# Kernel optimization log

Hardware: AMD Instinct MI355X
Metric: run time of the kernel (lower is better)

Reference implementation:

```python
import jax, jax.numpy as jnp
import numpy as np

INPUT_DIM = 1024
HIDDEN_DIM = 64  # per-head dim
NUM_HEADS = 16
LN_EPS = 1e-5


def setup_inputs() -> dict:
    key = jax.random.key(0)
    ks = jax.random.split(key, 12)
    B, S, D = 2, 2048, INPUT_DIM
    HD = HIDDEN_DIM * NUM_HEADS
    s_in = 1.0 / np.sqrt(D)
    s_hd = 1.0 / np.sqrt(HD)
    return {
        "x": jax.random.normal(ks[0], (B, S, D), dtype=jnp.float32),
        "Wq": jax.random.normal(ks[1], (D, HD), dtype=jnp.float32) * s_in,
        "bq": jax.random.normal(ks[2], (HD,), dtype=jnp.float32) * 0.02,
        "Wk": jax.random.normal(ks[3], (D, HD), dtype=jnp.float32) * s_in,
        "bk": jax.random.normal(ks[4], (HD,), dtype=jnp.float32) * 0.02,
        "Wv": jax.random.normal(ks[5], (D, HD), dtype=jnp.float32) * s_in,
        "bv": jax.random.normal(ks[6], (HD,), dtype=jnp.float32) * 0.02,
        "Wo": jax.random.normal(ks[7], (HD, D), dtype=jnp.float32) * s_hd,
        "bo": jax.random.normal(ks[8], (D,), dtype=jnp.float32) * 0.02,
        "gamma": jnp.ones((D,), dtype=jnp.float32),
        "beta": jnp.zeros((D,), dtype=jnp.float32),
    }


def _layer_norm(y, gamma, beta):
    mu = jnp.mean(y, axis=-1, keepdims=True)
    var = jnp.mean(jnp.square(y - mu), axis=-1, keepdims=True)
    return (y - mu) * jax.lax.rsqrt(var + LN_EPS) * gamma + beta


def reference(x, Wq, bq, Wk, bk, Wv, bv, Wo, bo, gamma, beta):
    B, S, D = x.shape
    H, Hd = NUM_HEADS, HIDDEN_DIM
    # Faithful to the torch module: (B,S,H*Hd) -> reshape (B,H,S,Hd) WITHOUT transpose.
    Q = (x @ Wq + bq).reshape(B, H, S, Hd)
    K = (x @ Wk + bk).reshape(B, H, S, Hd)
    V = (x @ Wv + bv).reshape(B, H, S, Hd)
    scores = jnp.einsum("bhqd,bhkd->bhqk", Q, K) / jnp.sqrt(jnp.float32(Hd))
    attn = jax.nn.softmax(scores, axis=-1)  # dropout=0 -> identity
    ctx = jnp.einsum("bhqk,bhkd->bhqd", attn, V).reshape(B, S, H * Hd)
    out = _layer_norm(x + (ctx @ Wo + bo), gamma, beta)
    return jax.nn.gelu(out, approximate=False)
```

## Files before the change

### kernel.cpp

```cpp
#include <hip/hip_runtime.h>
#include <hip/hip_bf16.h>
#include <cstdint>
#include <cstddef>


#define SEQ   2048
#define DIM   1024
#define NHEAD 16
#define HDIM  64
#define ROWS  4096

#define QSCALE 0.1803368801111204f

typedef __attribute__((ext_vector_type(8))) __bf16 bf16x8;
typedef __attribute__((ext_vector_type(4))) float floatx4;
typedef __attribute__((ext_vector_type(8))) unsigned short ushortx8;

__device__ __forceinline__ unsigned short f2bf(float f) {
  unsigned int u = __float_as_uint(f);
  u += 0x7FFFu + ((u >> 16) & 1u);
  return (unsigned short)(u >> 16);
}

__device__ __forceinline__ unsigned int pk2bf(float a, float b) {
  float2 f; f.x = a; f.y = b;
  __hip_bfloat162 h = __float22bfloat162_rn(f);
  return *(unsigned int*)&h;
}

__global__ __launch_bounds__(256) void cvt_bf16(const float* __restrict__ in,
                                                unsigned short* __restrict__ out,
                                                int n4) {
  int i = blockIdx.x * 256 + threadIdx.x;
  if (i >= n4) return;
  float4 v = ((const float4*)in)[i];
  ushort4 o;
  o.x = f2bf(v.x); o.y = f2bf(v.y); o.z = f2bf(v.z); o.w = f2bf(v.w);
  ((ushort4*)out)[i] = o;
}

__global__ __launch_bounds__(256) void transpose_w(const float* __restrict__ in,
                                                   unsigned short* __restrict__ out) {
  __shared__ float t[32][33];
  const int bx = blockIdx.x * 32, by = blockIdx.y * 32;
  const int tx = threadIdx.x, ty = threadIdx.y;
#pragma unroll
  for (int i = ty; i < 32; i += 8)
    t[i][tx] = in[(size_t)(by + i) * DIM + bx + tx];
  __syncthreads();
#pragma unroll
  for (int i = ty; i < 32; i += 8)
    out[(size_t)(bx + i) * DIM + by + tx] = f2bf(t[tx][i]);
}

__global__ __launch_bounds__(256) void transpose_v(
    const unsigned short* __restrict__ Vb,
    unsigned short* __restrict__ VbT) {
  __shared__ unsigned short t[64][65];
  const int bh = blockIdx.y;
  const int s0 = blockIdx.x * 64;
  const int tx = threadIdx.x;
  const int ty = threadIdx.y;
  const unsigned short* src = Vb + (size_t)bh * (SEQ * HDIM);
  unsigned short* dst = VbT + (size_t)bh * (SEQ * HDIM);
#pragma unroll
  for (int i = ty; i < 64; i += 4)
    t[i][tx] = src[(size_t)(s0 + i) * HDIM + tx];
  __syncthreads();
#pragma unroll
  for (int i = ty; i < 64; i += 4)
    dst[(size_t)i * SEQ + s0 + tx] = t[tx][i];
}

__global__ __launch_bounds__(256, 3) void gemm_qkv(
    const unsigned short* __restrict__ A,
    const unsigned short* __restrict__ Wt,
    const float* __restrict__ bq, const float* __restrict__ bk,
    const float* __restrict__ bv,
    unsigned short* __restrict__ Qb, unsigned short* __restrict__ Kb,
    unsigned short* __restrict__ Vb) {
  constexpr int K = DIM;
  __shared__ unsigned short As[128 * 72];
  __shared__ unsigned short Bs[128 * 72];
  const int tid  = threadIdx.x;
  const int lane = tid & 63, wave = tid >> 6;
  const int l16  = lane & 15, quad = lane >> 4;
  const int wm   = (wave & 1) * 64, wn = (wave >> 1) * 64;
  const int tm   = blockIdx.y * 128, tn = blockIdx.x * 128;
  const int srow = tid >> 3, scol = (tid & 7) * 8;

  floatx4 acc[4][4] = {};

  for (int k0 = 0; k0 < K; k0 += 64) {
    __syncthreads();
#pragma unroll
    for (int p = 0; p < 4; ++p) {
      const int row = srow + p * 32;
      *(ushortx8*)&As[row * 72 + scol] =
          *(const ushortx8*)&A[(size_t)(tm + row) * K + k0 + scol];
      *(ushortx8*)&Bs[row * 72 + scol] =
          *(const ushortx8*)&Wt[(size_t)(tn + row) * K + k0 + scol];
    }
    __syncthreads();
#pragma unroll
    for (int step = 0; step < 2; ++step) {
      const int kk = step * 32 + quad * 8;
      bf16x8 af[4], bfr[4];
#pragma unroll
      for (int i = 0; i < 4; ++i)
        af[i] = *(const bf16x8*)&As[(wm + i * 16 + l16) * 72 + kk];
#pragma unroll
      for (int j = 0; j < 4; ++j)
        bfr[j] = *(const bf16x8*)&Bs[(wn + j * 16 + l16) * 72 + kk];
#pragma unroll
      for (int i = 0; i < 4; ++i)
#pragma unroll
        for (int j = 0; j < 4; ++j)
          acc[i][j] = __builtin_amdgcn_mfma_f32_16x16x32_bf16(af[i], bfr[j],
                                                              acc[i][j], 0, 0, 0);
    }
  }

#pragma unroll
  for (int j = 0; j < 4; ++j) {
    const int ng  = tn + wn + j * 16 + l16;
    const int seg = ng >> 10;
    const int col = ng & 1023;
    const float* bp    = (seg == 0) ? bq : (seg == 1) ? bk : bv;
    unsigned short* op = (seg == 0) ? Qb : (seg == 1) ? Kb : Vb;
    const float bias = bp[col];
    const float scl  = (seg == 0) ? QSCALE : 1.0f;
#pragma unroll
    for (int i = 0; i < 4; ++i) {
      const int m0 = tm + wm + i * 16 + quad * 4;
#pragma unroll
      for (int r = 0; r < 4; ++r)
        op[(size_t)(m0 + r) * DIM + col] = f2bf((acc[i][j][r] + bias) * scl);
    }
  }
}

__global__ __launch_bounds__(256, 3) void gemm_o(
    const unsigned short* __restrict__ A,
    const unsigned short* __restrict__ Wt,
    const float* __restrict__ bo,
    float* __restrict__ Y) {
  constexpr int K = DIM;
  __shared__ unsigned short As[128 * 72];
  __shared__ unsigned short Bs[128 * 72];
  const int tid  = threadIdx.x;
  const int lane = tid & 63, wave = tid >> 6;
  const int l16  = lane & 15, quad = lane >> 4;
  const int wm   = (wave & 1) * 64, wn = (wave >> 1) * 64;
  const int tm   = blockIdx.y * 128, tn = blockIdx.x * 128;
  const int srow = tid >> 3, scol = (tid & 7) * 8;

  floatx4 acc[4][4] = {};

  for (int k0 = 0; k0 < K; k0 += 64) {
    __syncthreads();
#pragma unroll
    for (int p = 0; p < 4; ++p) {
      const int row = srow + p * 32;
      *(ushortx8*)&As[row * 72 + scol] =
          *(const ushortx8*)&A[(size_t)(tm + row) * K + k0 + scol];
      *(ushortx8*)&Bs[row * 72 + scol] =
          *(const ushortx8*)&Wt[(size_t)(tn + row) * K + k0 + scol];
    }
    __syncthreads();
#pragma unroll
    for (int step = 0; step < 2; ++step) {
      const int kk = step * 32 + quad * 8;
      bf16x8 af[4], bfr[4];
#pragma unroll
      for (int i = 0; i < 4; ++i)
        af[i] = *(const bf16x8*)&As[(wm + i * 16 + l16) * 72 + kk];
#pragma unroll
      for (int j = 0; j < 4; ++j)
        bfr[j] = *(const bf16x8*)&Bs[(wn + j * 16 + l16) * 72 + kk];
#pragma unroll
      for (int i = 0; i < 4; ++i)
#pragma unroll
        for (int j = 0; j < 4; ++j)
          acc[i][j] = __builtin_amdgcn_mfma_f32_16x16x32_bf16(af[i], bfr[j],
                                                              acc[i][j], 0, 0, 0);
    }
  }

#pragma unroll
  for (int j = 0; j < 4; ++j) {
    const int n = tn + wn + j * 16 + l16;
    const float bias = bo[n];
#pragma unroll
    for (int i = 0; i < 4; ++i) {
      const int m0 = tm + wm + i * 16 + quad * 4;
#pragma unroll
      for (int r = 0; r < 4; ++r)
        Y[(size_t)(m0 + r) * DIM + n] = acc[i][j][r] + bias;
    }
  }
}

__global__ __launch_bounds__(256, 2) void attn_fwd(
    const unsigned short* __restrict__ Qb,
    const unsigned short* __restrict__ Kb,
    const unsigned short* __restrict__ VbT,
    unsigned short* __restrict__ ctx) {
  __shared__ unsigned short Kl[64 * 72];
  __shared__ unsigned short Vt[64 * 72];
  __shared__ unsigned short Pl[4][32 * 72];

  const int tid  = threadIdx.x;
  const int lane = tid & 63, wave = tid >> 6;
  const int l16  = lane & 15, quad = lane >> 4;
  const size_t slab = (size_t)blockIdx.y * SEQ * HDIM;
  const unsigned short* Q  = Qb + slab;
  const unsigned short* Kp = Kb + slab;
  const unsigned short* Vp = VbT + slab;
  const int q0 = blockIdx.x * 128 + wave * 32;

  bf16x8 qf[2][2];
#pragma unroll
  for (int h = 0; h < 2; ++h) {
    qf[h][0] = *(const bf16x8*)&Q[(size_t)(q0 + h * 16 + l16) * HDIM + quad * 8];
    qf[h][1] = *(const bf16x8*)&Q[(size_t)(q0 + h * 16 + l16) * HDIM + 32 + quad * 8];
  }

  floatx4 o[2][4] = {};
  float lr[2] = {0.f, 0.f};

  const int srow = tid >> 3, scol = (tid & 7) * 8;

  for (int kt = 0; kt < SEQ; kt += 64) {
    __syncthreads();
#pragma unroll
    for (int p = 0; p < 2; ++p) {
      const int row = srow + p * 32;
      *(ushortx8*)&Kl[row * 72 + scol] =
          *(const ushortx8*)&Kp[(size_t)(kt + row) * HDIM + scol];
      *(ushortx8*)&Vt[row * 72 + scol] =
          *(const ushortx8*)&Vp[((size_t)row << 11) + kt + scol];
    }
    __syncthreads();

    floatx4 s[2][4] = {};
#pragma unroll
    for (int step = 0; step < 2; ++step) {
      const int kk = step * 32 + quad * 8;
#pragma unroll
      for (int mt = 0; mt < 4; ++mt) {
        bf16x8 kfr = *(const bf16x8*)&Kl[(mt * 16 + l16) * 72 + kk];
        s[0][mt] = __builtin_amdgcn_mfma_f32_16x16x32_bf16(kfr, qf[0][step], s[0][mt], 0, 0, 0);
        s[1][mt] = __builtin_amdgcn_mfma_f32_16x16x32_bf16(kfr, qf[1][step], s[1][mt], 0, 0, 0);
      }
    }

#pragma unroll
    for (int h = 0; h < 2; ++h) {
#pragma unroll
      for (int mt = 0; mt < 4; ++mt) {
        float p0 = __builtin_amdgcn_exp2f(s[h][mt][0]);
        float p1 = __builtin_amdgcn_exp2f(s[h][mt][1]);
        float p2 = __builtin_amdgcn_exp2f(s[h][mt][2]);
        float p3 = __builtin_amdgcn_exp2f(s[h][mt][3]);
        lr[h] += (p0 + p1) + (p2 + p3);
        uint2 pv;
        pv.x = pk2bf(p0, p1);
        pv.y = pk2bf(p2, p3);
        *(uint2*)&Pl[wave][(h * 16 + l16) * 72 + mt * 16 + quad * 4] = pv;
      }
    }
    __asm__ __volatile__("s_waitcnt lgkmcnt(0)" ::: "memory");

#pragma unroll
    for (int step = 0; step < 2; ++step) {
      const int kk = step * 32 + quad * 8;
      bf16x8 pf0 = *(const bf16x8*)&Pl[wave][(l16) * 72 + kk];
      bf16x8 pf1 = *(const bf16x8*)&Pl[wave][(16 + l16) * 72 + kk];
#pragma unroll
      for (int j = 0; j < 4; ++j) {
        bf16x8 vf = *(const bf16x8*)&Vt[(j * 16 + l16) * 72 + kk];
        o[0][j] = __builtin_amdgcn_mfma_f32_16x16x32_bf16(pf0, vf, o[0][j], 0, 0, 0);
        o[1][j] = __builtin_amdgcn_mfma_f32_16x16x32_bf16(pf1, vf, o[1][j], 0, 0, 0);
      }
    }
  }

#pragma unroll
  for (int h = 0; h < 2; ++h) {
    lr[h] += __shfl_xor(lr[h], 16, 64);
    lr[h] += __shfl_xor(lr[h], 32, 64);
  }
  unsigned short* cp = ctx + slab;
#pragma unroll
  for (int h = 0; h < 2; ++h) {
    float lb[4];
#pragma unroll
    for (int r = 0; r < 4; ++r)
      lb[r] = 1.0f / __shfl(lr[h], quad * 4 + r, 64);
#pragma unroll
    for (int j = 0; j < 4; ++j)
#pragma unroll
      for (int r = 0; r < 4; ++r)
        cp[(size_t)(q0 + h * 16 + quad * 4 + r) * HDIM + j * 16 + l16] =
            f2bf(o[h][j][r] * lb[r]);
  }
}

__global__ __launch_bounds__(256) void ln_gelu(
    const float* __restrict__ x, const float* __restrict__ y,
    const float* __restrict__ gamma, const float* __restrict__ beta,
    float* __restrict__ out) {
  const int row = blockIdx.x;
  const float* xr = x + (size_t)row * DIM;
  const float* yr = y + (size_t)row * DIM;
  float s[4];
  float sum = 0.f, sq = 0.f;
#pragma unroll
  for (int p = 0; p < 4; ++p) {
    const int c = p * 256 + threadIdx.x;
    s[p] = xr[c] + yr[c];
    sum += s[p];
    sq  += s[p] * s[p];
  }
#pragma unroll
  for (int off = 1; off < 64; off <<= 1) {
    sum += __shfl_xor(sum, off, 64);
    sq  += __shfl_xor(sq, off, 64);
  }
  __shared__ float red[8];
  const int wave = threadIdx.x >> 6, lane = threadIdx.x & 63;
  if (lane == 0) { red[wave] = sum; red[wave + 4] = sq; }
  __syncthreads();
  sum = red[0] + red[1] + red[2] + red[3];
  sq  = red[4] + red[5] + red[6] + red[7];
  const float mu   = sum * (1.0f / DIM);
  const float var  = sq * (1.0f / DIM) - mu * mu;
  const float rstd = rsqrtf(var + 1e-5f);
  float* orow = out + (size_t)row * DIM;
#pragma unroll
  for (int p = 0; p < 4; ++p) {
    const int c = p * 256 + threadIdx.x;
    const float v = (s[p] - mu) * rstd * gamma[c] + beta[c];
    orow[c] = 0.5f * v * (1.0f + erff(v * 0.70710678118654752f));
  }
}

extern "C" void kernel_launch(void* const* d_in, const int* in_sizes, int n_in,
                              void* d_out, int out_size, void* d_ws, size_t ws_size,
                              hipStream_t stream) {
  (void)in_sizes; (void)n_in; (void)out_size; (void)ws_size;
  const float* x     = (const float*)d_in[0];
  const float* Wq    = (const float*)d_in[1];
  const float* bq    = (const float*)d_in[2];
  const float* Wk    = (const float*)d_in[3];
  const float* bk    = (const float*)d_in[4];
  const float* Wv    = (const float*)d_in[5];
  const float* bv    = (const float*)d_in[6];
  const float* Wo    = (const float*)d_in[7];
  const float* bo    = (const float*)d_in[8];
  const float* gamma = (const float*)d_in[9];
  const float* beta  = (const float*)d_in[10];
  float* out = (float*)d_out;

  char* ws = (char*)d_ws;
  const size_t MB = 1u << 20;
  unsigned short* xb    = (unsigned short*)(ws);
  unsigned short* Wqkvt = (unsigned short*)(ws + 8 * MB);
  unsigned short* Wot   = (unsigned short*)(ws + 14 * MB);
  unsigned short* Qb    = (unsigned short*)(ws + 16 * MB);
  unsigned short* Kb    = (unsigned short*)(ws + 24 * MB);
  unsigned short* VbT   = (unsigned short*)(ws + 32 * MB);
  unsigned short* Vb    = (unsigned short*)(ws + 40 * MB);
  unsigned short* Cx    = (unsigned short*)(ws + 40 * MB);
  float*          Y     = (float*)(ws + 48 * MB);

  cvt_bf16<<<(ROWS * DIM / 4 + 255) / 256, 256, 0, stream>>>(x, xb, ROWS * DIM / 4);
  dim3 tb(32, 8), tg(32, 32);
  transpose_w<<<tg, tb, 0, stream>>>(Wq, Wqkvt);
  transpose_w<<<tg, tb, 0, stream>>>(Wk, Wqkvt + (size_t)DIM * DIM);
  transpose_w<<<tg, tb, 0, stream>>>(Wv, Wqkvt + 2 * (size_t)DIM * DIM);
  transpose_w<<<tg, tb, 0, stream>>>(Wo, Wot);

  gemm_qkv<<<dim3(24, 32), 256, 0, stream>>>(xb, Wqkvt, bq, bk, bv, Qb, Kb, Vb);
  transpose_v<<<dim3(SEQ / 64, 32), dim3(64, 4), 0, stream>>>(Vb, VbT);
  attn_fwd<<<dim3(16, 32), 256, 0, stream>>>(Qb, Kb, VbT, Cx);
  gemm_o<<<dim3(8, 32), 256, 0, stream>>>(Cx, Wot, bo, Y);
  ln_gelu<<<ROWS, 256, 0, stream>>>(x, Y, gamma, beta, out);
}
```

Measured before the change: 253.6 us.

## Use single-wave attention blocks, narrower O-GEMM tiles, one fused weight-transpose launch

The attention kernel now runs one 64-thread wave per block over 2048 blocks. Each wave loads its K and V fragments straight from global memory into registers instead of staging them in shared memory behind block barriers. Block indices are swizzled so neighbouring blocks share a head, which should improve L2 reuse of K/V. The output GEMM switches to 128x64 tiles (twice as many blocks, no occupancy hint), the four weight transposes become one launch, and LayerNorm+GELU uses float4 loads and stores. The trade-off is that every wave now refetches K/V through the cache rather than sharing one shared-memory copy, which raises global and L2 traffic.

```diff
diff --git a/kernel.cpp b/kernel.cpp
--- a/kernel.cpp
+++ b/kernel.cpp
@@ -39,9 +39,14 @@
   ((ushort4*)out)[i] = o;
 }
 
-__global__ __launch_bounds__(256) void transpose_w(const float* __restrict__ in,
-                                                   unsigned short* __restrict__ out) {
+__global__ __launch_bounds__(256) void transpose_w4(
+    const float* __restrict__ Wq, const float* __restrict__ Wk,
+    const float* __restrict__ Wv, const float* __restrict__ Wo,
+    unsigned short* __restrict__ Wqkvt, unsigned short* __restrict__ Wot) {
   __shared__ float t[32][33];
+  const int z = blockIdx.z;
+  const float* in = (z == 0) ? Wq : (z == 1) ? Wk : (z == 2) ? Wv : Wo;
+  unsigned short* out = (z < 3) ? Wqkvt + (size_t)z * DIM * DIM : Wot;
   const int bx = blockIdx.x * 32, by = blockIdx.y * 32;
   const int tx = threadIdx.x, ty = threadIdx.y;
 #pragma unroll
@@ -140,22 +145,22 @@
   }
 }
 
-__global__ __launch_bounds__(256, 3) void gemm_o(
+__global__ __launch_bounds__(256) void gemm_o(
     const unsigned short* __restrict__ A,
     const unsigned short* __restrict__ Wt,
     const float* __restrict__ bo,
     float* __restrict__ Y) {
   constexpr int K = DIM;
   __shared__ unsigned short As[128 * 72];
-  __shared__ unsigned short Bs[128 * 72];
+  __shared__ unsigned short Bs[64 * 72];
   const int tid  = threadIdx.x;
   const int lane = tid & 63, wave = tid >> 6;
   const int l16  = lane & 15, quad = lane >> 4;
-  const int wm   = (wave & 1) * 64, wn = (wave >> 1) * 64;
-  const int tm   = blockIdx.y * 128, tn = blockIdx.x * 128;
+  const int wm   = wave * 32;
+  const int tm   = blockIdx.y * 128, tn = blockIdx.x * 64;
   const int srow = tid >> 3, scol = (tid & 7) * 8;
 
-  floatx4 acc[4][4] = {};
+  floatx4 acc[2][4] = {};
 
   for (int k0 = 0; k0 < K; k0 += 64) {
     __syncthreads();
@@ -164,22 +169,27 @@
       const int row = srow + p * 32;
       *(ushortx8*)&As[row * 72 + scol] =
           *(const ushortx8*)&A[(size_t)(tm + row) * K + k0 + scol];
-      *(ushortx8*)&Bs[row * 72 + scol] =
-          *(const ushortx8*)&Wt[(size_t)(tn + row) * K + k0 + scol];
+    }
+#pragma unroll
+    for (int p = 0; p < 2; ++p) {
+      const int row = srow + p * 32;
+      if (row < 64)
+        *(ushortx8*)&Bs[row * 72 + scol] =
+            *(const ushortx8*)&Wt[(size_t)(tn + row) * K + k0 + scol];
     }
     __syncthreads();
 #pragma unroll
     for (int step = 0; step < 2; ++step) {
       const int kk = step * 32 + quad * 8;
-      bf16x8 af[4], bfr[4];
-#pragma unroll
-      for (int i = 0; i < 4; ++i)
+      bf16x8 af[2], bfr[4];
+#pragma unroll
+      for (int i = 0; i < 2; ++i)
         af[i] = *(const bf16x8*)&As[(wm + i * 16 + l16) * 72 + kk];
 #pragma unroll
       for (int j = 0; j < 4; ++j)
-        bfr[j] = *(const bf16x8*)&Bs[(wn + j * 16 + l16) * 72 + kk];
-#pragma unroll
-      for (int i = 0; i < 4; ++i)
+        bfr[j] = *(const bf16x8*)&Bs[(j * 16 + l16) * 72 + kk];
+#pragma unroll
+      for (int i = 0; i < 2; ++i)
 #pragma unroll
         for (int j = 0; j < 4; ++j)
           acc[i][j] = __builtin_amdgcn_mfma_f32_16x16x32_bf16(af[i], bfr[j],
@@ -189,10 +199,10 @@
 
 #pragma unroll
   for (int j = 0; j < 4; ++j) {
-    const int n = tn + wn + j * 16 + l16;
+    const int n = tn + j * 16 + l16;
     const float bias = bo[n];
 #pragma unroll
-    for (int i = 0; i < 4; ++i) {
+    for (int i = 0; i < 2; ++i) {
       const int m0 = tm + wm + i * 16 + quad * 4;
 #pragma unroll
       for (int r = 0; r < 4; ++r)
@@ -201,23 +211,23 @@
   }
 }
 
-__global__ __launch_bounds__(256, 2) void attn_fwd(
+__global__ __launch_bounds__(64) void attn_fwd(
     const unsigned short* __restrict__ Qb,
     const unsigned short* __restrict__ Kb,
     const unsigned short* __restrict__ VbT,
     unsigned short* __restrict__ ctx) {
-  __shared__ unsigned short Kl[64 * 72];
-  __shared__ unsigned short Vt[64 * 72];
-  __shared__ unsigned short Pl[4][32 * 72];
-
-  const int tid  = threadIdx.x;
-  const int lane = tid & 63, wave = tid >> 6;
+  __shared__ unsigned short Pl[32 * 72];
+
+  const int lane = threadIdx.x;
   const int l16  = lane & 15, quad = lane >> 4;
-  const size_t slab = (size_t)blockIdx.y * SEQ * HDIM;
+  const int b    = blockIdx.x;
+  const int bh   = (b >> 3) & 31;
+  const int qt   = ((b >> 8) << 3) | (b & 7);
+  const size_t slab = (size_t)bh * SEQ * HDIM;
   const unsigned short* Q  = Qb + slab;
   const unsigned short* Kp = Kb + slab;
   const unsigned short* Vp = VbT + slab;
-  const int q0 = blockIdx.x * 128 + wave * 32;
+  const int q0 = qt * 32;
 
   bf16x8 qf[2][2];
 #pragma unroll
@@ -229,31 +239,29 @@
   floatx4 o[2][4] = {};
   float lr[2] = {0.f, 0.f};
 
-  const int srow = tid >> 3, scol = (tid & 7) * 8;
-
   for (int kt = 0; kt < SEQ; kt += 64) {
-    __syncthreads();
-#pragma unroll
-    for (int p = 0; p < 2; ++p) {
-      const int row = srow + p * 32;
-      *(ushortx8*)&Kl[row * 72 + scol] =
-          *(const ushortx8*)&Kp[(size_t)(kt + row) * HDIM + scol];
-      *(ushortx8*)&Vt[row * 72 + scol] =
-          *(const ushortx8*)&Vp[((size_t)row << 11) + kt + scol];
-    }
-    __syncthreads();
+    bf16x8 kf[2][4], vf[2][4];
+#pragma unroll
+    for (int step = 0; step < 2; ++step)
+#pragma unroll
+      for (int mt = 0; mt < 4; ++mt)
+        kf[step][mt] = *(const bf16x8*)
+            &Kp[(size_t)(kt + mt * 16 + l16) * HDIM + step * 32 + quad * 8];
+#pragma unroll
+    for (int step = 0; step < 2; ++step)
+#pragma unroll
+      for (int j = 0; j < 4; ++j)
+        vf[step][j] = *(const bf16x8*)
+            &Vp[((size_t)(j * 16 + l16) << 11) + kt + step * 32 + quad * 8];
 
     floatx4 s[2][4] = {};
 #pragma unroll
-    for (int step = 0; step < 2; ++step) {
-      const int kk = step * 32 + quad * 8;
+    for (int step = 0; step < 2; ++step)
 #pragma unroll
       for (int mt = 0; mt < 4; ++mt) {
-        bf16x8 kfr = *(const bf16x8*)&Kl[(mt * 16 + l16) * 72 + kk];
-        s[0][mt] = __builtin_amdgcn_mfma_f32_16x16x32_bf16(kfr, qf[0][step], s[0][mt], 0, 0, 0);
-        s[1][mt] = __builtin_amdgcn_mfma_f32_16x16x32_bf16(kfr, qf[1][step], s[1][mt], 0, 0, 0);
+        s[0][mt] = __builtin_amdgcn_mfma_f32_16x16x32_bf16(kf[step][mt], qf[0][step], s[0][mt], 0, 0, 0);
+        s[1][mt] = __builtin_amdgcn_mfma_f32_16x16x32_bf16(kf[step][mt], qf[1][step], s[1][mt], 0, 0, 0);
       }
-    }
 
 #pragma unroll
     for (int h = 0; h < 2; ++h) {
@@ -267,7 +275,7 @@
         uint2 pv;
         pv.x = pk2bf(p0, p1);
         pv.y = pk2bf(p2, p3);
-        *(uint2*)&Pl[wave][(h * 16 + l16) * 72 + mt * 16 + quad * 4] = pv;
+        *(uint2*)&Pl[(h * 16 + l16) * 72 + mt * 16 + quad * 4] = pv;
       }
     }
     __asm__ __volatile__("s_waitcnt lgkmcnt(0)" ::: "memory");
@@ -275,13 +283,12 @@
 #pragma unroll
     for (int step = 0; step < 2; ++step) {
       const int kk = step * 32 + quad * 8;
-      bf16x8 pf0 = *(const bf16x8*)&Pl[wave][(l16) * 72 + kk];
-      bf16x8 pf1 = *(const bf16x8*)&Pl[wave][(16 + l16) * 72 + kk];
+      bf16x8 pf0 = *(const bf16x8*)&Pl[(l16) * 72 + kk];
+      bf16x8 pf1 = *(const bf16x8*)&Pl[(16 + l16) * 72 + kk];
 #pragma unroll
       for (int j = 0; j < 4; ++j) {
-        bf16x8 vf = *(const bf16x8*)&Vt[(j * 16 + l16) * 72 + kk];
-        o[0][j] = __builtin_amdgcn_mfma_f32_16x16x32_bf16(pf0, vf, o[0][j], 0, 0, 0);
-        o[1][j] = __builtin_amdgcn_mfma_f32_16x16x32_bf16(pf1, vf, o[1][j], 0, 0, 0);
+        o[0][j] = __builtin_amdgcn_mfma_f32_16x16x32_bf16(pf0, vf[step][j], o[0][j], 0, 0, 0);
+        o[1][j] = __builtin_amdgcn_mfma_f32_16x16x32_bf16(pf1, vf[step][j], o[1][j], 0, 0, 0);
       }
     }
   }
@@ -312,24 +319,20 @@
     const float* __restrict__ gamma, const float* __restrict__ beta,
     float* __restrict__ out) {
   const int row = blockIdx.x;
-  const float* xr = x + (size_t)row * DIM;
-  const float* yr = y + (size_t)row * DIM;
-  float s[4];
-  float sum = 0.f, sq = 0.f;
-#pragma unroll
-  for (int p = 0; p < 4; ++p) {
-    const int c = p * 256 + threadIdx.x;
-    s[p] = xr[c] + yr[c];
-    sum += s[p];
-    sq  += s[p] * s[p];
-  }
+  const int tid = threadIdx.x;
+  const float4 xv = ((const float4*)(x + (size_t)row * DIM))[tid];
+  const float4 yv = ((const float4*)(y + (size_t)row * DIM))[tid];
+  float4 s;
+  s.x = xv.x + yv.x; s.y = xv.y + yv.y; s.z = xv.z + yv.z; s.w = xv.w + yv.w;
+  float sum = (s.x + s.y) + (s.z + s.w);
+  float sq  = (s.x * s.x + s.y * s.y) + (s.z * s.z + s.w * s.w);
 #pragma unroll
   for (int off = 1; off < 64; off <<= 1) {
     sum += __shfl_xor(sum, off, 64);
     sq  += __shfl_xor(sq, off, 64);
   }
   __shared__ float red[8];
-  const int wave = threadIdx.x >> 6, lane = threadIdx.x & 63;
+  const int wave = tid >> 6, lane = tid & 63;
   if (lane == 0) { red[wave] = sum; red[wave + 4] = sq; }
   __syncthreads();
   sum = red[0] + red[1] + red[2] + red[3];
@@ -337,13 +340,26 @@
   const float mu   = sum * (1.0f / DIM);
   const float var  = sq * (1.0f / DIM) - mu * mu;
   const float rstd = rsqrtf(var + 1e-5f);
-  float* orow = out + (size_t)row * DIM;
-#pragma unroll
-  for (int p = 0; p < 4; ++p) {
-    const int c = p * 256 + threadIdx.x;
-    const float v = (s[p] - mu) * rstd * gamma[c] + beta[c];
-    orow[c] = 0.5f * v * (1.0f + erff(v * 0.70710678118654752f));
-  }
+  const float4 gv = ((const float4*)gamma)[tid];
+  const float4 bv = ((const float4*)beta)[tid];
+  float4 ov;
+  {
+    const float v = (s.x - mu) * rstd * gv.x + bv.x;
+    ov.x = 0.5f * v * (1.0f + erff(v * 0.70710678118654752f));
+  }
+  {
+    const float v = (s.y - mu) * rstd * gv.y + bv.y;
+    ov.y = 0.5f * v * (1.0f + erff(v * 0.70710678118654752f));
+  }
+  {
+    const float v = (s.z - mu) * rstd * gv.z + bv.z;
+    ov.z = 0.5f * v * (1.0f + erff(v * 0.70710678118654752f));
+  }
+  {
+    const float v = (s.w - mu) * rstd * gv.w + bv.w;
+    ov.w = 0.5f * v * (1.0f + erff(v * 0.70710678118654752f));
+  }
+  ((float4*)(out + (size_t)row * DIM))[tid] = ov;
 }
 
 extern "C" void kernel_launch(void* const* d_in, const int* in_sizes, int n_in,
@@ -376,15 +392,11 @@
   float*          Y     = (float*)(ws + 48 * MB);
 
   cvt_bf16<<<(ROWS * DIM / 4 + 255) / 256, 256, 0, stream>>>(x, xb, ROWS * DIM / 4);
-  dim3 tb(32, 8), tg(32, 32);
-  transpose_w<<<tg, tb, 0, stream>>>(Wq, Wqkvt);
-  transpose_w<<<tg, tb, 0, stream>>>(Wk, Wqkvt + (size_t)DIM * DIM);
-  transpose_w<<<tg, tb, 0, stream>>>(Wv, Wqkvt + 2 * (size_t)DIM * DIM);
-  transpose_w<<<tg, tb, 0, stream>>>(Wo, Wot);
+  transpose_w4<<<dim3(32, 32, 4), dim3(32, 8), 0, stream>>>(Wq, Wk, Wv, Wo, Wqkvt, Wot);
 
   gemm_qkv<<<dim3(24, 32), 256, 0, stream>>>(xb, Wqkvt, bq, bk, bv, Qb, Kb, Vb);
   transpose_v<<<dim3(SEQ / 64, 32), dim3(64, 4), 0, stream>>>(Vb, VbT);
-  attn_fwd<<<dim3(16, 32), 256, 0, stream>>>(Qb, Kb, VbT, Cx);
-  gemm_o<<<dim3(8, 32), 256, 0, stream>>>(Cx, Wot, bo, Y);
+  attn_fwd<<<2048, 64, 0, stream>>>(Qb, Kb, VbT, Cx);
+  gemm_o<<<dim3(16, 32), 256, 0, stream>>>(Cx, Wot, bo, Y);
   ln_gelu<<<ROWS, 256, 0, stream>>>(x, Y, gamma, beta, out);
 }
```

Result: slower. 297.3 us (+17.2%).
